# Kernel optimization log

Hardware: AMD Instinct MI355X
Metric: run time of the kernel (lower is better)

Reference implementation:

```python
import jax, jax.numpy as jnp
import numpy as np

D_MODEL, D_HEAD, N_HEADS, N_KV_HEADS = 4096, 128, 32, 8
EPS = 1e-5
N = 2048


def rms_norm(x, w, eps):
    return x * jax.lax.rsqrt(jnp.mean(x * x, axis=-1, keepdims=True) + eps) * w


def rope_swap(x):
    # [x0, x1, x2, x3] -> [-x1, x0, -x3, x2]
    xp = x.reshape(x.shape[:-1] + (-1, 2))
    return jnp.stack([-xp[..., 1], xp[..., 0]], axis=-1).reshape(x.shape)


def rope_rotate(x, r_cos, r_sin):
    return x * r_cos + rope_swap(x) * r_sin


def setup_inputs() -> dict:
    key = jax.random.key(0)
    ks = jax.random.split(key, 8)
    sd = 1.0 / np.sqrt(D_MODEL)
    return {
        "x": jax.random.normal(ks[0], (N, D_MODEL), dtype=jnp.float32),
        "r_cos": jax.random.normal(ks[1], (N, D_HEAD), dtype=jnp.float32),
        "r_sin": jax.random.normal(ks[2], (N, D_HEAD), dtype=jnp.float32),
        "w_norm": jnp.ones((D_MODEL,), dtype=jnp.float32),
        "wq": jax.random.normal(ks[3], (D_MODEL, N_HEADS * D_HEAD), dtype=jnp.float32) * sd,
        "wk": jax.random.normal(ks[4], (D_MODEL, N_KV_HEADS * D_HEAD), dtype=jnp.float32) * sd,
        "wv": jax.random.normal(ks[5], (D_MODEL, N_KV_HEADS * D_HEAD), dtype=jnp.float32) * sd,
        "wo": jax.random.normal(ks[6], (D_MODEL, D_MODEL), dtype=jnp.float32) * sd,
    }


def reference(x, r_cos, r_sin, w_norm, wq, wk, wv, wo):
    n = x.shape[0]
    residual = x
    h = rms_norm(x, w_norm, EPS)

    # projections -> [n_heads, n, d_head]
    q = (h @ wq).reshape(n, N_HEADS, D_HEAD).transpose(1, 0, 2)
    k = (h @ wk).reshape(n, N_KV_HEADS, D_HEAD).transpose(1, 0, 2)
    v = (h @ wv).reshape(n, N_KV_HEADS, D_HEAD).transpose(1, 0, 2)

    # GQA: repeat kv heads
    reps = N_HEADS // N_KV_HEADS
    k = jnp.repeat(k, reps, axis=0)
    v = jnp.repeat(v, reps, axis=0)

    q = rope_rotate(q, r_cos, r_sin)
    k = rope_rotate(k, r_cos, r_sin)

    mask = jnp.where(
        jnp.tril(jnp.ones((n, n), dtype=bool)), 0.0, -jnp.inf
    ).astype(x.dtype)
    scores = jnp.einsum("hnd,hmd->hnm", q, k) / np.sqrt(D_HEAD).astype(np.float32) + mask
    a = jnp.einsum("hnm,hmd->hnd", jax.nn.softmax(scores, axis=-1), v)

    a = a.transpose(1, 0, 2).reshape(n, N_HEADS * D_HEAD)
    return residual + a @ wo
```

## Files before the change

kernel.cpp:

```cpp
#include <hip/hip_runtime.h>
#include <stdint.h>
#include <math.h>

#define TOK 2048
#define DMODEL 4096
#define QKV_LD 5120
#define KVB 64
#define PS_LD 72

typedef __attribute__((ext_vector_type(8))) short short8;
typedef __attribute__((ext_vector_type(4))) short short4v;
typedef __attribute__((ext_vector_type(8))) __bf16 bf16x8;
typedef __attribute__((ext_vector_type(4))) float f32x4;

__device__ __forceinline__ unsigned short f2bf(float f) {
  unsigned u = __float_as_uint(f);
  u += 0x7fffu + ((u >> 16) & 1u);
  return (unsigned short)(u >> 16);
}

__device__ __forceinline__ void gl16(const void* g, void* l) {
  __builtin_amdgcn_global_load_lds((__attribute__((address_space(1))) void*)g,
                                   (__attribute__((address_space(3))) void*)l,
                                   16, 0, 0);
}

__device__ __forceinline__ f32x4 mfma16(short8 a, short8 b, f32x4 c) {
  return __builtin_amdgcn_mfma_f32_16x16x32_bf16(__builtin_bit_cast(bf16x8, a),
                                                 __builtin_bit_cast(bf16x8, b),
                                                 c, 0, 0, 0);
}

__device__ __forceinline__ float fexp2(float x) {
  float r;
  asm("v_exp_f32 %0, %1" : "=v"(r) : "v"(x));
  return r;
}

__device__ __forceinline__ void waitvm0() {
  asm volatile("s_waitcnt vmcnt(0)" ::: "memory");
}

__global__ __launch_bounds__(256) void k_rmsnorm(const float* __restrict__ x,
                                                 const float* __restrict__ w,
                                                 unsigned short* __restrict__ h) {
  const int row = blockIdx.x;
  const float* xr = x + (size_t)row * DMODEL;
  float4 v[4];
  float ss = 0.f;
#pragma unroll
  for (int i = 0; i < 4; ++i) {
    v[i] = *(const float4*)(xr + threadIdx.x * 4 + i * 1024);
    ss += v[i].x * v[i].x + v[i].y * v[i].y + v[i].z * v[i].z + v[i].w * v[i].w;
  }
#pragma unroll
  for (int m = 1; m < 64; m <<= 1) ss += __shfl_xor(ss, m, 64);
  __shared__ float ws4[4];
  if ((threadIdx.x & 63) == 0) ws4[threadIdx.x >> 6] = ss;
  __syncthreads();
  const float scale = rsqrtf((ws4[0] + ws4[1] + ws4[2] + ws4[3]) * (1.0f / DMODEL) + 1e-5f);
  unsigned short* hr = h + (size_t)row * DMODEL;
#pragma unroll
  for (int i = 0; i < 4; ++i) {
    int col = threadIdx.x * 4 + i * 1024;
    float4 wv = *(const float4*)(w + col);
    uint2 o;
    o.x = (unsigned)f2bf(v[i].x * scale * wv.x) | ((unsigned)f2bf(v[i].y * scale * wv.y) << 16);
    o.y = (unsigned)f2bf(v[i].z * scale * wv.z) | ((unsigned)f2bf(v[i].w * scale * wv.w) << 16);
    *(uint2*)(hr + col) = o;
  }
}

__global__ __launch_bounds__(256) void k_wconvert(const float* __restrict__ W,
                                                  unsigned short* __restrict__ WT,
                                                  int K, int N) {
  __shared__ unsigned short tile[64][65];
  const int n0 = blockIdx.x * 64, k0 = blockIdx.y * 64;
  const int t = threadIdx.x;
  {
    const int r = t >> 2, c0 = (t & 3) * 16;
    const float* src = W + (size_t)(k0 + r) * N + n0 + c0;
#pragma unroll
    for (int i = 0; i < 4; ++i) {
      float4 f = *(const float4*)(src + i * 4);
      tile[r][c0 + i * 4 + 0] = f2bf(f.x);
      tile[r][c0 + i * 4 + 1] = f2bf(f.y);
      tile[r][c0 + i * 4 + 2] = f2bf(f.z);
      tile[r][c0 + i * 4 + 3] = f2bf(f.w);
    }
  }
  __syncthreads();
  {
    const int n = t >> 2, c0 = (t & 3) * 16;
    unsigned short* dst = WT + (size_t)(n0 + n) * K + k0 + c0;
    unsigned short v[16];
#pragma unroll
    for (int i = 0; i < 16; ++i) v[i] = tile[c0 + i][n];
    uint4 o0, o1;
    o0.x = v[0] | ((unsigned)v[1] << 16);  o0.y = v[2] | ((unsigned)v[3] << 16);
    o0.z = v[4] | ((unsigned)v[5] << 16);  o0.w = v[6] | ((unsigned)v[7] << 16);
    o1.x = v[8] | ((unsigned)v[9] << 16);  o1.y = v[10] | ((unsigned)v[11] << 16);
    o1.z = v[12] | ((unsigned)v[13] << 16); o1.w = v[14] | ((unsigned)v[15] << 16);
    *(uint4*)dst = o0;
    *(uint4*)(dst + 8) = o1;
  }
}

__device__ __forceinline__ short8 rdfrag(const unsigned short* buf, int row, int kc) {
  return *(const short8*)((const char*)buf + row * 128 + ((kc ^ (row & 7)) << 4));
}

template <int BM, int BN>
__device__ __forceinline__ void stage_tile(const unsigned short* __restrict__ A,
                                           const unsigned short* __restrict__ BT,
                                           unsigned short* __restrict__ buf,
                                           int m0, int n0, int K, int kt, int tid) {
  constexpr int LA = BM / 64, LB = BN / 64;
  unsigned short* bbuf = buf + BM * 64;
#pragma unroll
  for (int i = 0; i < LA; ++i) {
    const int s = i * 512 + tid, row = s >> 3, ch = s & 7;
    gl16(A + (size_t)(m0 + row) * K + kt + ((ch ^ (row & 7)) << 3), (char*)buf + s * 16);
  }
#pragma unroll
  for (int i = 0; i < LB; ++i) {
    const int s = i * 512 + tid, row = s >> 3, ch = s & 7;
    gl16(BT + (size_t)(n0 + row) * K + kt + ((ch ^ (row & 7)) << 3), (char*)bbuf + s * 16);
  }
}

template <int BM, int BN, int MODE, int LOGN>
__global__ __launch_bounds__(512, 2) void k_gemm_big(const unsigned short* __restrict__ A,
                                                     const unsigned short* __restrict__ BT,
                                                     const float* __restrict__ resid,
                                                     void* __restrict__ Cout,
                                                     unsigned short* __restrict__ vtg,
                                                     const float* __restrict__ rc,
                                                     const float* __restrict__ rs,
                                                     int M, int N, int K) {
  extern __shared__ __align__(16) unsigned short lds[];
  constexpr int MREP = BM / 32;
  constexpr int NREP = BN / 64;
  constexpr int MH = MREP / 2;
  constexpr int TILE = (BM + BN) * 64;

  const int tid = threadIdx.x, lane = tid & 63;
  const int w = tid >> 6, wm = w >> 2, wn = w & 3;
  const int lr = lane & 15, lh = lane >> 4;

  const int wg0 = blockIdx.x;
  const int xcd = wg0 & 7, l = wg0 >> 3;
  const int mch = (M / BM) >> 1;
  const int m0 = ((xcd >> 2) * mch + (l >> LOGN)) * BM;
  const int n0 = ((xcd & 3) * (1 << LOGN) + (l & ((1 << LOGN) - 1))) * BN;

  const f32x4 zf = {0.f, 0.f, 0.f, 0.f};
  f32x4 acc[MREP][NREP];
#pragma unroll
  for (int i = 0; i < MREP; ++i) {
#pragma unroll
    for (int j = 0; j < NREP; ++j) acc[i][j] = zf;
  }

  const int arow0 = wm * (BM / 2);
  const int brow0 = wn * (BN / 4);
  const int NT = K >> 6;
  int cur = 0;

  stage_tile<BM, BN>(A, BT, lds, m0, n0, K, 0, tid);

  for (int t = 0; t < NT; ++t) {
    const unsigned short* abuf = lds + cur * TILE;
    const unsigned short* bbuf = abuf + BM * 64;
    waitvm0();
    __builtin_amdgcn_s_barrier();
    __builtin_amdgcn_sched_barrier(0);
    if (t + 1 < NT)
      stage_tile<BM, BN>(A, BT, lds + (cur ^ 1) * TILE, m0, n0, K, (t + 1) << 6, tid);

#pragma unroll
    for (int kk = 0; kk < 2; ++kk) {
      short8 bfr[NREP];
#pragma unroll
      for (int nr = 0; nr < NREP; ++nr)
        bfr[nr] = rdfrag(bbuf, brow0 + nr * 16 + lr, kk * 4 + lh);
#pragma unroll
      for (int mh = 0; mh < 2; ++mh) {
        short8 afr[MH];
#pragma unroll
        for (int mi = 0; mi < MH; ++mi)
          afr[mi] = rdfrag(abuf, arow0 + (mh * MH + mi) * 16 + lr, kk * 4 + lh);
        __builtin_amdgcn_s_setprio(1);
#pragma unroll
        for (int mi = 0; mi < MH; ++mi) {
#pragma unroll
          for (int nr = 0; nr < NREP; ++nr)
            acc[mh * MH + mi][nr] = mfma16(afr[mi], bfr[nr], acc[mh * MH + mi][nr]);
        }
        __builtin_amdgcn_s_setprio(0);
      }
    }
    cur ^= 1;
  }

#pragma unroll
  for (int ai = 0; ai < MREP; ++ai) {
#pragma unroll
    for (int ni = 0; ni < NREP; ++ni) {
      const int colg = n0 + wn * (BN / 4) + ni * 16 + lr;
      const int rowg0 = m0 + wm * (BM / 2) + ai * 16 + 4 * lh;
      if (MODE == 1) {
#pragma unroll
        for (int r = 0; r < 4; ++r)
          ((float*)Cout)[(size_t)(rowg0 + r) * N + colg] =
              acc[ai][ni][r] + resid[(size_t)(rowg0 + r) * N + colg];
      } else if (colg >= 5120) {
        short4v o;
#pragma unroll
        for (int r = 0; r < 4; ++r) o[r] = (short)f2bf(acc[ai][ni][r]);
        *(short4v*)(vtg + (size_t)(colg - 5120) * TOK + rowg0) = o;
      } else {
        const int d = colg & 127;
#pragma unroll
        for (int r = 0; r < 4; ++r) {
          const int row = rowg0 + r;
          const float v = acc[ai][ni][r];
          const float p = __shfl_xor(v, 1, 64);
          const float c = rc[row * 128 + d];
          const float s = rs[row * 128 + d];
          const float y = (lr & 1) ? fmaf(p, s, v * c) : fmaf(-p, s, v * c);
          ((unsigned short*)Cout)[(size_t)row * QKV_LD + colg] = f2bf(y);
        }
      }
    }
  }
}

__global__ __launch_bounds__(256) void k_attn(const unsigned short* __restrict__ qkv,
                                              const unsigned short* __restrict__ vtg,
                                              unsigned short* __restrict__ aout) {
  extern __shared__ __align__(16) unsigned short sm[];
  unsigned short* const KsB = sm;
  unsigned short* const VtB = sm + 2 * KVB * 128;
  unsigned short* const Ps = sm + 4 * KVB * 128;
  const int head = blockIdx.y;
  const int hkv = head >> 2;
  const int tid = threadIdx.x, lane = tid & 63, w = tid >> 6;
  const int lr = lane & 15, lh = lane >> 4;
  const float scale2 = 0.08838834764831845f * 1.44269504088896340736f;
  const f32x4 zf = {0.f, 0.f, 0.f, 0.f};

  auto stageKV = [&](int kvt, int buf) {
    unsigned short* Ksn = KsB + buf * (KVB * 128);
    unsigned short* Vtn = VtB + buf * (128 * KVB);
    const int kvn = kvt * KVB;
#pragma unroll
    for (int c = 0; c < 4; ++c) {
      const int s = c * 256 + w * 64 + lane;
      const int row = s >> 4, cp = s & 15;
      gl16(qkv + (size_t)(kvn + row) * QKV_LD + 4096 + hkv * 128 + ((cp ^ (row & 7)) * 8),
           (char*)Ksn + (c * 256 + w * 64) * 16);
    }
#pragma unroll
    for (int c = 0; c < 4; ++c) {
      const int s = c * 256 + w * 64 + lane;
      const int row = s >> 3, cp = s & 7;
      gl16(vtg + (size_t)(hkv * 128 + row) * TOK + kvn + ((cp ^ (row & 7)) * 8),
           (char*)Vtn + (c * 256 + w * 64) * 16);
    }
  };

  for (int half = 0; half < 2; ++half) {
    const int qt = half ? (31 - blockIdx.x) : blockIdx.x;
    const int q0 = qt * 64;

    short8 qf[4];
    {
      const unsigned short* qbase = qkv + (size_t)(q0 + w * 16 + lr) * QKV_LD + head * 128;
#pragma unroll
      for (int kd = 0; kd < 4; ++kd) qf[kd] = *(const short8*)(qbase + kd * 32 + lh * 8);
    }
    f32x4 oacc[8];
#pragma unroll
    for (int vt = 0; vt < 8; ++vt) oacc[vt] = zf;
    float Mr[4], Lp[4];
#pragma unroll
    for (int r = 0; r < 4; ++r) { Mr[r] = -INFINITY; Lp[r] = 0.f; }

    const int nt = qt + 1;
    int cur = 0;
    stageKV(0, 0);

    for (int t = 0; t < nt; ++t) {
      const unsigned short* Ks = KsB + cur * (KVB * 128);
      const unsigned short* Vt = VtB + cur * (128 * KVB);
      const int kv0 = t * KVB;
      waitvm0();
      __builtin_amdgcn_s_barrier();
      __builtin_amdgcn_sched_barrier(0);
      if (t + 1 < nt) stageKV(t + 1, cur ^ 1);

      f32x4 sacc[4];
#pragma unroll
      for (int ct = 0; ct < 4; ++ct) {
        sacc[ct] = zf;
        const int row = ct * 16 + lr;
#pragma unroll
        for (int kd = 0; kd < 4; ++kd) {
          const short8 kf = *(const short8*)((const char*)Ks + row * 256 +
                                             (((kd * 4 + lh) ^ (row & 7)) * 16));
          sacc[ct] = mfma16(qf[kd], kf, sacc[ct]);
        }
      }

      const bool diag = (t == qt);
      float sv[4][4], gmax[4];
#pragma unroll
      for (int r = 0; r < 4; ++r) {
        float s0 = sacc[0][r] * scale2;
        float s1 = sacc[1][r] * scale2;
        float s2 = sacc[2][r] * scale2;
        float s3 = sacc[3][r] * scale2;
        if (diag) {
          const int qrow = q0 + w * 16 + 4 * lh + r;
          if (kv0 + lr > qrow) s0 = -INFINITY;
          if (kv0 + 16 + lr > qrow) s1 = -INFINITY;
          if (kv0 + 32 + lr > qrow) s2 = -INFINITY;
          if (kv0 + 48 + lr > qrow) s3 = -INFINITY;
        }
        float tmax = fmaxf(fmaxf(s0, s1), fmaxf(s2, s3));
        tmax = fmaxf(tmax, __shfl_xor(tmax, 1, 16));
        tmax = fmaxf(tmax, __shfl_xor(tmax, 2, 16));
        tmax = fmaxf(tmax, __shfl_xor(tmax, 4, 16));
        tmax = fmaxf(tmax, __shfl_xor(tmax, 8, 16));
        gmax[r] = tmax;
        sv[r][0] = s0; sv[r][1] = s1; sv[r][2] = s2; sv[r][3] = s3;
      }
      const int cond = (gmax[0] <= Mr[0] + 8.f) && (gmax[1] <= Mr[1] + 8.f) &&
                       (gmax[2] <= Mr[2] + 8.f) && (gmax[3] <= Mr[3] + 8.f);
      if (!__all(cond)) {
        float scv[4];
#pragma unroll
        for (int r = 0; r < 4; ++r) {
          const float mnew = fmaxf(Mr[r], gmax[r]);
          scv[r] = fexp2(Mr[r] - mnew);
          Mr[r] = mnew;
          Lp[r] *= scv[r];
        }
#pragma unroll
        for (int vt = 0; vt < 8; ++vt) {
#pragma unroll
          for (int r = 0; r < 4; ++r) oacc[vt][r] *= scv[r];
        }
      }
      float pv[4][4];
#pragma unroll
      for (int r = 0; r < 4; ++r) {
        const float p0 = fexp2(sv[r][0] - Mr[r]);
        const float p1 = fexp2(sv[r][1] - Mr[r]);
        const float p2 = fexp2(sv[r][2] - Mr[r]);
        const float p3 = fexp2(sv[r][3] - Mr[r]);
        Lp[r] += (p0 + p1) + (p2 + p3);
        pv[r][0] = p0; pv[r][1] = p1; pv[r][2] = p2; pv[r][3] = p3;
      }

      unsigned short* pw = Ps + w * (16 * PS_LD);
#pragma unroll
      for (int r = 0; r < 4; ++r) {
#pragma unroll
        for (int ct = 0; ct < 4; ++ct)
          pw[(4 * lh + r) * PS_LD + ct * 16 + lr] = f2bf(pv[r][ct]);
      }
      asm volatile("s_waitcnt lgkmcnt(0)" ::: "memory");
      short8 pf[2];
      pf[0] = *(const short8*)(pw + lr * PS_LD + lh * 8);
      pf[1] = *(const short8*)(pw + lr * PS_LD + 32 + lh * 8);
      __builtin_amdgcn_s_setprio(1);
#pragma unroll
      for (int vt = 0; vt < 8; ++vt) {
        const int d = vt * 16 + lr;
#pragma unroll
        for (int kb = 0; kb < 2; ++kb) {
          const short8 vf = *(const short8*)((const char*)Vt + d * 128 +
                                             (((kb * 4 + lh) ^ (lr & 7)) * 16));
          oacc[vt] = mfma16(pf[kb], vf, oacc[vt]);
        }
      }
      __builtin_amdgcn_s_setprio(0);
      cur ^= 1;
    }

#pragma unroll
    for (int r = 0; r < 4; ++r) {
      float Ls = Lp[r];
      Ls += __shfl_xor(Ls, 1, 16);
      Ls += __shfl_xor(Ls, 2, 16);
      Ls += __shfl_xor(Ls, 4, 16);
      Ls += __shfl_xor(Ls, 8, 16);
      const float inv = 1.0f / Ls;
      const size_t rowoff = (size_t)(q0 + w * 16 + 4 * lh + r) * DMODEL + head * 128;
#pragma unroll
      for (int vt = 0; vt < 8; ++vt)
        aout[rowoff + vt * 16 + lr] = f2bf(oacc[vt][r] * inv);
    }
    __builtin_amdgcn_s_barrier();
    __builtin_amdgcn_sched_barrier(0);
  }
}

extern "C" void kernel_launch(void* const* d_in, const int* in_sizes, int n_in,
                              void* d_out, int out_size, void* d_ws, size_t ws_size,
                              hipStream_t stream) {
  (void)in_sizes; (void)n_in; (void)out_size; (void)ws_size;
  const float* x     = (const float*)d_in[0];
  const float* r_cos = (const float*)d_in[1];
  const float* r_sin = (const float*)d_in[2];
  const float* wnorm = (const float*)d_in[3];
  const float* wq    = (const float*)d_in[4];
  const float* wk    = (const float*)d_in[5];
  const float* wv    = (const float*)d_in[6];
  const float* wo    = (const float*)d_in[7];

  unsigned short* bufA = (unsigned short*)d_ws;
  unsigned short* qkvb = bufA + (size_t)TOK * DMODEL;
  unsigned short* wT   = qkvb + (size_t)TOK * QKV_LD;
  unsigned short* vtg  = wT + (size_t)6144 * DMODEL;

  hipFuncSetAttribute((const void*)k_gemm_big<256, 192, 0, 3>,
                      hipFuncAttributeMaxDynamicSharedMemorySize, 4 * (256 + 192) * 64);
  hipFuncSetAttribute((const void*)k_gemm_big<128, 256, 1, 2>,
                      hipFuncAttributeMaxDynamicSharedMemorySize, 4 * (128 + 256) * 64);
  const int attn_lds = 4 * KVB * 128 * 2 + 4 * 16 * PS_LD * 2;
  hipFuncSetAttribute((const void*)k_attn,
                      hipFuncAttributeMaxDynamicSharedMemorySize, attn_lds);

  k_rmsnorm<<<TOK, 256, 0, stream>>>(x, wnorm, bufA);
  k_wconvert<<<dim3(64, 64), 256, 0, stream>>>(wq, wT, DMODEL, 4096);
  k_wconvert<<<dim3(16, 64), 256, 0, stream>>>(wk, wT + (size_t)4096 * DMODEL, DMODEL, 1024);
  k_wconvert<<<dim3(16, 64), 256, 0, stream>>>(wv, wT + (size_t)5120 * DMODEL, DMODEL, 1024);
  k_gemm_big<256, 192, 0, 3><<<dim3(256), 512, 4 * (256 + 192) * 64, stream>>>(
      bufA, wT, nullptr, qkvb, vtg, r_cos, r_sin, TOK, 6144, DMODEL);
  k_wconvert<<<dim3(64, 64), 256, 0, stream>>>(wo, wT, DMODEL, 4096);
  k_attn<<<dim3(16, 32), 256, attn_lds, stream>>>(qkvb, vtg, bufA);
  k_gemm_big<128, 256, 1, 2><<<dim3(256), 512, 4 * (128 + 256) * 64, stream>>>(
      bufA, wT, x, d_out, nullptr, nullptr, nullptr, TOK, DMODEL, DMODEL);
}
```

Measured before the change: 309.0 us.

## Restructure GEMM main loop into four barrier-separated phases with split prefetch

The GEMM inner loop is split into four phases (two k-steps times two M halves). Each phase loads its LDS fragments, issues half of the next tile's global-to-LDS prefetch in the first two phases, then runs its MFMAs between barriers, with a vmcnt wait only at the end. The goal is to interleave global loads and LDS reads with MFMA work more evenly across warps, the usual ping-pong style schedule. The output projection GEMM also changes tile shape from 128x256 to 256x128, and the workgroup-to-tile mapping is hardcoded to a fixed 8-column XCD layout in place of the LOGN template. The extra barriers add synchronisation cost.

```diff
diff --git a/kernel.cpp b/kernel.cpp
--- a/kernel.cpp
+++ b/kernel.cpp
@@ -110,26 +110,57 @@
   return *(const short8*)((const char*)buf + row * 128 + ((kc ^ (row & 7)) << 4));
 }
 
-template <int BM, int BN>
-__device__ __forceinline__ void stage_tile(const unsigned short* __restrict__ A,
+template <int BM, int BN, int HALF>
+__device__ __forceinline__ void stage_half(const unsigned short* __restrict__ A,
                                            const unsigned short* __restrict__ BT,
                                            unsigned short* __restrict__ buf,
                                            int m0, int n0, int K, int kt, int tid) {
   constexpr int LA = BM / 64, LB = BN / 64;
+  constexpr int H0A = LA / 2, H0B = (LB + 1) / 2;
+  constexpr int A0 = HALF ? H0A : 0, A1 = HALF ? LA : H0A;
+  constexpr int B0 = HALF ? H0B : 0, B1 = HALF ? LB : H0B;
   unsigned short* bbuf = buf + BM * 64;
 #pragma unroll
-  for (int i = 0; i < LA; ++i) {
+  for (int i = A0; i < A1; ++i) {
     const int s = i * 512 + tid, row = s >> 3, ch = s & 7;
     gl16(A + (size_t)(m0 + row) * K + kt + ((ch ^ (row & 7)) << 3), (char*)buf + s * 16);
   }
 #pragma unroll
-  for (int i = 0; i < LB; ++i) {
+  for (int i = B0; i < B1; ++i) {
     const int s = i * 512 + tid, row = s >> 3, ch = s & 7;
     gl16(BT + (size_t)(n0 + row) * K + kt + ((ch ^ (row & 7)) << 3), (char*)bbuf + s * 16);
   }
 }
 
-template <int BM, int BN, int MODE, int LOGN>
+#define GPHASE(KK, MG, STG, LASTP)                                             \
+  {                                                                            \
+    if ((MG) == 0) {                                                           \
+      _Pragma("unroll")                                                        \
+      for (int nr = 0; nr < NREP; ++nr)                                        \
+        bfr[nr] = rdfrag(bbuf, brow0 + nr * 16 + lr, (KK) * 4 + lh);           \
+    }                                                                          \
+    short8 afr[4];                                                             \
+    _Pragma("unroll")                                                          \
+    for (int mi = 0; mi < 4; ++mi)                                             \
+      afr[mi] = rdfrag(abuf, arow0 + ((MG) * 4 + mi) * 16 + lr, (KK) * 4 + lh);\
+    if ((STG) == 1 && pre) stage_half<BM, BN, 0>(A, BT, nbuf, m0, n0, K, ktn, tid); \
+    if ((STG) == 2 && pre) stage_half<BM, BN, 1>(A, BT, nbuf, m0, n0, K, ktn, tid); \
+    __builtin_amdgcn_s_barrier();                                              \
+    asm volatile("s_waitcnt lgkmcnt(0)" ::: "memory");                         \
+    __builtin_amdgcn_sched_barrier(0);                                         \
+    __builtin_amdgcn_s_setprio(1);                                             \
+    _Pragma("unroll")                                                          \
+    for (int mi = 0; mi < 4; ++mi) {                                           \
+      _Pragma("unroll")                                                        \
+      for (int nr = 0; nr < NREP; ++nr)                                        \
+        acc[(MG) * 4 + mi][nr] = mfma16(afr[mi], bfr[nr], acc[(MG) * 4 + mi][nr]); \
+    }                                                                          \
+    __builtin_amdgcn_s_setprio(0);                                             \
+    if (LASTP) asm volatile("s_waitcnt vmcnt(0)" ::: "memory");                \
+    __builtin_amdgcn_s_barrier();                                              \
+  }
+
+template <int BM, int BN, int MODE>
 __global__ __launch_bounds__(512, 2) void k_gemm_big(const unsigned short* __restrict__ A,
                                                      const unsigned short* __restrict__ BT,
                                                      const float* __restrict__ resid,
@@ -141,7 +172,6 @@
   extern __shared__ __align__(16) unsigned short lds[];
   constexpr int MREP = BM / 32;
   constexpr int NREP = BN / 64;
-  constexpr int MH = MREP / 2;
   constexpr int TILE = (BM + BN) * 64;
 
   const int tid = threadIdx.x, lane = tid & 63;
@@ -150,9 +180,8 @@
 
   const int wg0 = blockIdx.x;
   const int xcd = wg0 & 7, l = wg0 >> 3;
-  const int mch = (M / BM) >> 1;
-  const int m0 = ((xcd >> 2) * mch + (l >> LOGN)) * BM;
-  const int n0 = ((xcd & 3) * (1 << LOGN) + (l & ((1 << LOGN) - 1))) * BN;
+  const int m0 = (((xcd >> 2) << 2) + (l >> 3)) * BM;
+  const int n0 = (((xcd & 3) << 3) + (l & 7)) * BN;
 
   const f32x4 zf = {0.f, 0.f, 0.f, 0.f};
   f32x4 acc[MREP][NREP];
@@ -167,39 +196,23 @@
   const int NT = K >> 6;
   int cur = 0;
 
-  stage_tile<BM, BN>(A, BT, lds, m0, n0, K, 0, tid);
+  stage_half<BM, BN, 0>(A, BT, lds, m0, n0, K, 0, tid);
+  stage_half<BM, BN, 1>(A, BT, lds, m0, n0, K, 0, tid);
+  waitvm0();
+  __builtin_amdgcn_s_barrier();
 
   for (int t = 0; t < NT; ++t) {
     const unsigned short* abuf = lds + cur * TILE;
     const unsigned short* bbuf = abuf + BM * 64;
-    waitvm0();
-    __builtin_amdgcn_s_barrier();
-    __builtin_amdgcn_sched_barrier(0);
-    if (t + 1 < NT)
-      stage_tile<BM, BN>(A, BT, lds + (cur ^ 1) * TILE, m0, n0, K, (t + 1) << 6, tid);
-
-#pragma unroll
-    for (int kk = 0; kk < 2; ++kk) {
-      short8 bfr[NREP];
-#pragma unroll
-      for (int nr = 0; nr < NREP; ++nr)
-        bfr[nr] = rdfrag(bbuf, brow0 + nr * 16 + lr, kk * 4 + lh);
-#pragma unroll
-      for (int mh = 0; mh < 2; ++mh) {
-        short8 afr[MH];
-#pragma unroll
-        for (int mi = 0; mi < MH; ++mi)
-          afr[mi] = rdfrag(abuf, arow0 + (mh * MH + mi) * 16 + lr, kk * 4 + lh);
-        __builtin_amdgcn_s_setprio(1);
-#pragma unroll
-        for (int mi = 0; mi < MH; ++mi) {
-#pragma unroll
-          for (int nr = 0; nr < NREP; ++nr)
-            acc[mh * MH + mi][nr] = mfma16(afr[mi], bfr[nr], acc[mh * MH + mi][nr]);
-        }
-        __builtin_amdgcn_s_setprio(0);
-      }
-    }
+    unsigned short* nbuf = lds + (cur ^ 1) * TILE;
+    const bool pre = (t + 1 < NT);
+    const int ktn = (t + 1) << 6;
+
+    short8 bfr[NREP];
+    GPHASE(0, 0, 1, 0)
+    GPHASE(0, 1, 2, 0)
+    GPHASE(1, 0, 0, 0)
+    GPHASE(1, 1, 0, 1)
     cur ^= 1;
   }
 
@@ -426,10 +439,10 @@
   unsigned short* wT   = qkvb + (size_t)TOK * QKV_LD;
   unsigned short* vtg  = wT + (size_t)6144 * DMODEL;
 
-  hipFuncSetAttribute((const void*)k_gemm_big<256, 192, 0, 3>,
+  hipFuncSetAttribute((const void*)k_gemm_big<256, 192, 0>,
                       hipFuncAttributeMaxDynamicSharedMemorySize, 4 * (256 + 192) * 64);
-  hipFuncSetAttribute((const void*)k_gemm_big<128, 256, 1, 2>,
-                      hipFuncAttributeMaxDynamicSharedMemorySize, 4 * (128 + 256) * 64);
+  hipFuncSetAttribute((const void*)k_gemm_big<256, 128, 1>,
+                      hipFuncAttributeMaxDynamicSharedMemorySize, 4 * (256 + 128) * 64);
   const int attn_lds = 4 * KVB * 128 * 2 + 4 * 16 * PS_LD * 2;
   hipFuncSetAttribute((const void*)k_attn,
                       hipFuncAttributeMaxDynamicSharedMemorySize, attn_lds);
@@ -438,10 +451,10 @@
   k_wconvert<<<dim3(64, 64), 256, 0, stream>>>(wq, wT, DMODEL, 4096);
   k_wconvert<<<dim3(16, 64), 256, 0, stream>>>(wk, wT + (size_t)4096 * DMODEL, DMODEL, 1024);
   k_wconvert<<<dim3(16, 64), 256, 0, stream>>>(wv, wT + (size_t)5120 * DMODEL, DMODEL, 1024);
-  k_gemm_big<256, 192, 0, 3><<<dim3(256), 512, 4 * (256 + 192) * 64, stream>>>(
+  k_gemm_big<256, 192, 0><<<dim3(256), 512, 4 * (256 + 192) * 64, stream>>>(
       bufA, wT, nullptr, qkvb, vtg, r_cos, r_sin, TOK, 6144, DMODEL);
   k_wconvert<<<dim3(64, 64), 256, 0, stream>>>(wo, wT, DMODEL, 4096);
   k_attn<<<dim3(16, 32), 256, attn_lds, stream>>>(qkvb, vtg, bufA);
-  k_gemm_big<128, 256, 1, 2><<<dim3(256), 512, 4 * (128 + 256) * 64, stream>>>(
+  k_gemm_big<256, 128, 1><<<dim3(256), 512, 4 * (256 + 128) * 64, stream>>>(
       bufA, wT, x, d_out, nullptr, nullptr, nullptr, TOK, DMODEL, DMODEL);
 }
```

Measured after the change: 314.8 us. No clear change (+1.9%).
